# Kernel tuning notes

Hardware: AMD Instinct MI355X
Metric: run time of the kernel (lower is better)

## Reference

```python
import jax, jax.numpy as jnp
import numpy as np

D_IN = 768
D_OUT = 768
NUM_HEADS = 12
HEAD_DIM = D_OUT // NUM_HEADS


def setup_inputs() -> dict:
    key = jax.random.key(0)
    ks = jax.random.split(key, 6)
    s = 1.0 / np.sqrt(D_IN)
    X = jax.random.normal(ks[0], (4, 2048, D_IN), dtype=jnp.float32)
    Wq = jax.random.uniform(ks[1], (D_IN, D_OUT), jnp.float32, -s, s)
    Wk = jax.random.uniform(ks[2], (D_IN, D_OUT), jnp.float32, -s, s)
    Wv = jax.random.uniform(ks[3], (D_IN, D_OUT), jnp.float32, -s, s)
    Wo = jax.random.uniform(ks[4], (D_OUT, D_OUT), jnp.float32, -s, s)
    bo = jax.random.uniform(ks[5], (D_OUT,), jnp.float32, -s, s)
    return {"X": X, "Wq": Wq, "Wk": Wk, "Wv": Wv, "Wo": Wo, "bo": bo}


def reference(X, Wq, Wk, Wv, Wo, bo):
    b, n, _ = X.shape
    # QKV projections, split heads -> [b, h, n, d]
    def split(t):
        return t.reshape(b, n, NUM_HEADS, HEAD_DIM).transpose(0, 2, 1, 3)
    q = split(X @ Wq)
    k = split(X @ Wk)
    v = split(X @ Wv)
    scores = jnp.einsum('bhqd,bhkd->bhqk', q, k) / np.sqrt(HEAD_DIM).astype(np.float32)
    causal = jnp.triu(jnp.ones((n, n), dtype=bool), k=1)
    scores = jnp.where(causal, -jnp.inf, scores)
    attn = jax.nn.softmax(scores, axis=-1)  # dropout p=0 -> identity
    ctx = jnp.einsum('bhqk,bhkd->bhqd', attn, v)
    ctx = ctx.transpose(0, 2, 1, 3).reshape(b, n, D_OUT)
    return ctx @ Wo + bo
```

## Files before the change

kernel.cpp:

```cpp
#include <hip/hip_runtime.h>
#include <stdint.h>

#define B_  4
#define N_  2048
#define D_  768
#define H_  12
#define HD_ 64
#define M_  (B_*N_)

typedef short bf8 __attribute__((ext_vector_type(8)));
typedef float f32x4 __attribute__((ext_vector_type(4)));

static __device__ __forceinline__ unsigned short f2bf(float f) {
    unsigned u = __float_as_uint(f);
    unsigned r = u + 0x7fffu + ((u >> 16) & 1u);
    return (unsigned short)(r >> 16);
}

static __device__ __forceinline__ unsigned pk2bf(float f0, float f1) {
    return ((__float_as_uint(f1) + 0x8000u) & 0xFFFF0000u) |
           ((__float_as_uint(f0) + 0x8000u) >> 16);
}

#if __has_builtin(__builtin_amdgcn_exp2f)
#define EXP2(x) __builtin_amdgcn_exp2f(x)
#else
#define EXP2(x) exp2f(x)
#endif

#define GLOAD_LDS16(gptr, lptr)                                                   \
    __builtin_amdgcn_global_load_lds(                                             \
        (const __attribute__((address_space(1))) void*)(gptr),                    \
        (__attribute__((address_space(3))) void*)(lptr), 16, 0, 0)

#define QSCALE 0.1803368801111204f

__global__ __launch_bounds__(256) void convert_x(const float* __restrict__ X,
                                                 unsigned short* __restrict__ Xb) {
    const size_t i = ((size_t)blockIdx.x * 256 + threadIdx.x) * 8;
    const float4 a = *(const float4*)(X + i);
    const float4 b = *(const float4*)(X + i + 4);
    ushort4 lo, hi;
    lo.x = f2bf(a.x); lo.y = f2bf(a.y); lo.z = f2bf(a.z); lo.w = f2bf(a.w);
    hi.x = f2bf(b.x); hi.y = f2bf(b.y); hi.z = f2bf(b.z); hi.w = f2bf(b.w);
    *(ushort4*)(Xb + i)     = lo;
    *(ushort4*)(Xb + i + 4) = hi;
}

__global__ __launch_bounds__(256) void transpose_w(
    const float* __restrict__ Wq, const float* __restrict__ Wk,
    const float* __restrict__ Wv, const float* __restrict__ Wo,
    unsigned short* __restrict__ Wqt, unsigned short* __restrict__ Wkt,
    unsigned short* __restrict__ Wvt, unsigned short* __restrict__ Wot)
{
    __shared__ float tile[32][33];
    const int z = blockIdx.z;
    const float* W = (z == 0) ? Wq : (z == 1) ? Wk : (z == 2) ? Wv : Wo;
    unsigned short* Wt = (z == 0) ? Wqt : (z == 1) ? Wkt : (z == 2) ? Wvt : Wot;
    const int k0 = blockIdx.x * 32, n0 = blockIdx.y * 32;
    const int tx = threadIdx.x & 31, ty = threadIdx.x >> 5;
    #pragma unroll
    for (int i = 0; i < 4; ++i)
        tile[ty + 8 * i][tx] = W[(size_t)(k0 + ty + 8 * i) * D_ + n0 + tx];
    __syncthreads();
    #pragma unroll
    for (int i = 0; i < 4; ++i)
        Wt[(size_t)(n0 + ty + 8 * i) * D_ + k0 + tx] = f2bf(tile[tx][ty + 8 * i]);
}

__global__ __launch_bounds__(256) void qkv_mfma(
    const unsigned short* __restrict__ Xb,
    const unsigned short* __restrict__ Wqt, const unsigned short* __restrict__ Wkt,
    const unsigned short* __restrict__ Wvt,
    unsigned short* __restrict__ Qb, unsigned short* __restrict__ Kb,
    unsigned short* __restrict__ Vt)
{
    __shared__ unsigned short As[2][8192];
    __shared__ unsigned short Bs[2][8192];

    const int t = threadIdx.x;
    const int wave = t >> 6, lane = t & 63;
    const int col = lane & 15, quad = lane >> 4;
    const int wm = (wave & 1) * 64, wn = (wave >> 1) * 64;

    const int orig = blockIdx.x;
    const int wgid = (orig & 7) * 144 + (orig >> 3);
    const int m0  = (wgid / 18) * 128;
    const int nm  = wgid % 18;
    const int mat = nm / 6;
    const int n0  = (nm % 6) * 128;
    const unsigned short* Wt = (mat == 0) ? Wqt : (mat == 1) ? Wkt : Wvt;
    const bool sw = (mat != 2);

    const unsigned short* Ag = Xb + (size_t)(m0 + (t >> 2)) * D_ + (t & 3) * 8;
    const unsigned short* Bg = Wt + (size_t)(n0 + (t >> 2)) * D_ + (t & 3) * 8;
    unsigned short* AsD = &As[0][0] + t * 8;
    unsigned short* BsD = &Bs[0][0] + t * 8;

#define QKV_STAGE(bsel, kk)                                                        \
    do {                                                                           \
        GLOAD_LDS16(Ag + (kk),                        AsD + (bsel) * 8192);        \
        GLOAD_LDS16(Ag + (kk) + 32,                   AsD + (bsel) * 8192 + 4096); \
        GLOAD_LDS16(Ag + (size_t)64 * D_ + (kk),      AsD + (bsel) * 8192 + 2048); \
        GLOAD_LDS16(Ag + (size_t)64 * D_ + (kk) + 32, AsD + (bsel) * 8192 + 6144); \
        GLOAD_LDS16(Bg + (kk),                        BsD + (bsel) * 8192);        \
        GLOAD_LDS16(Bg + (kk) + 32,                   BsD + (bsel) * 8192 + 4096); \
        GLOAD_LDS16(Bg + (size_t)64 * D_ + (kk),      BsD + (bsel) * 8192 + 2048); \
        GLOAD_LDS16(Bg + (size_t)64 * D_ + (kk) + 32, BsD + (bsel) * 8192 + 6144); \
    } while (0)

    f32x4 acc[4][4] = {};

    QKV_STAGE(0, 0);
    asm volatile("s_waitcnt vmcnt(0)" ::: "memory");
    __builtin_amdgcn_s_barrier();
    __builtin_amdgcn_sched_barrier(0);

    #pragma unroll 2
    for (int it = 0; it < 12; ++it) {
        const int cur = it & 1;
        if (it + 1 < 12) QKV_STAGE(cur ^ 1, (it + 1) * 64);

        const unsigned short* Ab = &As[cur][0];
        const unsigned short* Bb = &Bs[cur][0];
        #pragma unroll
        for (int ks = 0; ks < 2; ++ks) {
            bf8 a[4], b[4];
            #pragma unroll
            for (int i = 0; i < 4; ++i)
                a[i] = *(const bf8*)(Ab + ks * 4096 + (wm + i * 16 + col) * 32 + quad * 8);
            #pragma unroll
            for (int j = 0; j < 4; ++j)
                b[j] = *(const bf8*)(Bb + ks * 4096 + (wn + j * 16 + col) * 32 + quad * 8);
            if (sw) {
                #pragma unroll
                for (int i = 0; i < 4; ++i)
                    #pragma unroll
                    for (int j = 0; j < 4; ++j)
                        acc[i][j] = __builtin_amdgcn_mfma_f32_16x16x32_bf16(b[j], a[i], acc[i][j], 0, 0, 0);
            } else {
                #pragma unroll
                for (int i = 0; i < 4; ++i)
                    #pragma unroll
                    for (int j = 0; j < 4; ++j)
                        acc[i][j] = __builtin_amdgcn_mfma_f32_16x16x32_bf16(a[i], b[j], acc[i][j], 0, 0, 0);
            }
        }

        asm volatile("s_waitcnt vmcnt(0)" ::: "memory");
        __builtin_amdgcn_s_barrier();
        __builtin_amdgcn_sched_barrier(0);
    }
#undef QKV_STAGE

    if (sw) {
        unsigned short* Out = (mat == 0) ? Qb : Kb;
        const float qsc = (mat == 0) ? QSCALE : 1.0f;
        #pragma unroll
        for (int i = 0; i < 4; ++i) {
            const int token = m0 + wm + i * 16 + col;
            const int bb = token >> 11, nn = token & (N_ - 1);
            #pragma unroll
            for (int j = 0; j < 4; ++j) {
                const int n = n0 + wn + j * 16 + quad * 4;
                const int h = n >> 6, d = n & 63;
                ushort4 pk;
                pk.x = f2bf(acc[i][j][0] * qsc);
                pk.y = f2bf(acc[i][j][1] * qsc);
                pk.z = f2bf(acc[i][j][2] * qsc);
                pk.w = f2bf(acc[i][j][3] * qsc);
                *(ushort4*)(Out + ((size_t)(bb * H_ + h) * N_ + nn) * HD_ + d) = pk;
            }
        }
    } else {
        #pragma unroll
        for (int j = 0; j < 4; ++j) {
            const int n = n0 + wn + j * 16 + col;
            const int h = n >> 6, d = n & 63;
            #pragma unroll
            for (int i = 0; i < 4; ++i) {
                const int mb = m0 + wm + i * 16 + quad * 4;
                const int bb = mb >> 11;
                const int nn = mb & (N_ - 1);
                const int nnp = (nn & ~31) | ((quad >> 1) << 4) | ((quad & 1) << 3) |
                                ((i & 1) << 2);
                ushort4 pk;
                pk.x = f2bf(acc[i][j][0]); pk.y = f2bf(acc[i][j][1]);
                pk.z = f2bf(acc[i][j][2]); pk.w = f2bf(acc[i][j][3]);
                *(ushort4*)(Vt + ((size_t)(bb * H_ + h) * HD_ + d) * N_ + nnp) = pk;
            }
        }
    }
}

static __device__ __forceinline__ void qk_mfma8(
    const bf8 (&ka)[4][2], bf8 qb0, bf8 qb1, f32x4 (&s)[4])
{
    __builtin_amdgcn_s_setprio(1);
    #pragma unroll
    for (int kc = 0; kc < 4; ++kc) {
        s[kc] = __builtin_amdgcn_mfma_f32_16x16x32_bf16(ka[kc][0], qb0, s[kc], 0, 0, 0);
        s[kc] = __builtin_amdgcn_mfma_f32_16x16x32_bf16(ka[kc][1], qb1, s[kc], 0, 0, 0);
    }
    __builtin_amdgcn_s_setprio(0);
}

static __device__ __forceinline__ void softmax_pack(
    const f32x4 (&s)[4], int k0, int q, bool mask, float& lpart,
    bf8& pb0, bf8& pb1, int quad)
{
    float p[4][4];
    if (mask) {
        #pragma unroll
        for (int kc = 0; kc < 4; ++kc)
            #pragma unroll
            for (int r = 0; r < 4; ++r) {
                const int key = k0 + kc * 16 + quad * 4 + r;
                p[kc][r] = EXP2((key > q) ? -INFINITY : s[kc][r]);
            }
    } else {
        #pragma unroll
        for (int kc = 0; kc < 4; ++kc)
            #pragma unroll
            for (int r = 0; r < 4; ++r) p[kc][r] = EXP2(s[kc][r]);
    }

    #pragma unroll
    for (int kc = 0; kc < 4; ++kc)
        #pragma unroll
        for (int r = 0; r < 4; ++r) lpart += p[kc][r];

    uint4 u0, u1;
    u0.x = pk2bf(p[0][0], p[0][1]); u0.y = pk2bf(p[0][2], p[0][3]);
    u0.z = pk2bf(p[1][0], p[1][1]); u0.w = pk2bf(p[1][2], p[1][3]);
    u1.x = pk2bf(p[2][0], p[2][1]); u1.y = pk2bf(p[2][2], p[2][3]);
    u1.z = pk2bf(p[3][0], p[3][1]); u1.w = pk2bf(p[3][2], p[3][3]);
    pb0 = *(bf8*)&u0;
    pb1 = *(bf8*)&u1;
}

static __device__ __forceinline__ void pv_acc(
    bf8 pb0, bf8 pb1, const bf8 (&va)[4][2], f32x4 (&o)[4])
{
    __builtin_amdgcn_s_setprio(1);
    #pragma unroll
    for (int dc = 0; dc < 4; ++dc) {
        o[dc] = __builtin_amdgcn_mfma_f32_16x16x32_bf16(va[dc][0], pb0, o[dc], 0, 0, 0);
        o[dc] = __builtin_amdgcn_mfma_f32_16x16x32_bf16(va[dc][1], pb1, o[dc], 0, 0, 0);
    }
    __builtin_amdgcn_s_setprio(0);
}

__global__ __launch_bounds__(256, 3) void attn_mfma(
    const unsigned short* __restrict__ Qb,
    const unsigned short* __restrict__ Kb,
    const unsigned short* __restrict__ Vt,
    unsigned short* __restrict__ Ctxb)
{
    __shared__ unsigned short Kl[2][64 * 64];
    __shared__ unsigned short Vl[2][64 * 64];

    const int t = threadIdx.x;
    const int wave = t >> 6;
    const int lane = t & 63;
    const int col  = lane & 15;
    const int quad = lane >> 4;

    const int orig = blockIdx.x;
    const int bid  = (orig & 7) * 96 + (orig >> 3);
    const int bh  = bid >> 4;
    const int x   = bid & 15;
    const int tl  = x, th = 31 - x;
    const int q0L = tl * 64 + wave * 16;
    const int q0H = th * 64 + wave * 16;
    const int qL  = q0L + col;
    const int qH  = q0H + col;

    const unsigned short* Kp = Kb + (size_t)bh * N_ * HD_;
    const unsigned short* Vp = Vt + (size_t)bh * HD_ * N_;
    const unsigned short* QpL = Qb + ((size_t)bh * N_ + q0L) * HD_;
    const unsigned short* QpH = Qb + ((size_t)bh * N_ + q0H) * HD_;

    const bf8 qbL0 = *(const bf8*)(QpL + (size_t)col * HD_ + quad * 8);
    const bf8 qbL1 = *(const bf8*)(QpL + (size_t)col * HD_ + 32 + quad * 8);
    const bf8 qbH0 = *(const bf8*)(QpH + (size_t)col * HD_ + quad * 8);
    const bf8 qbH1 = *(const bf8*)(QpH + (size_t)col * HD_ + 32 + quad * 8);

    f32x4 oL[4] = {}, oH[4] = {};
    float lL = 0.f, lH = 0.f;

    const int srow = t >> 3;
    const int gcol = (t & 7) ^ (srow & 7);
    const unsigned short* Kg = Kp + (size_t)srow * HD_ + gcol * 8;
    const unsigned short* Vg = Vp + (size_t)srow * N_ + gcol * 8;
    unsigned short* KlD = &Kl[0][0] + t * 8;
    unsigned short* VlD = &Vl[0][0] + t * 8;

#define ATT_STAGE(bsel, kt_)                                                       \
    do {                                                                           \
        GLOAD_LDS16(Kg + (size_t)(kt_) * 64 * HD_,        KlD + (bsel) * 4096);    \
        GLOAD_LDS16(Kg + (size_t)((kt_) * 64 + 32) * HD_, KlD + (bsel) * 4096 + 2048); \
        GLOAD_LDS16(Vg + (kt_) * 64,                      VlD + (bsel) * 4096);    \
        GLOAD_LDS16(Vg + (size_t)32 * N_ + (kt_) * 64,    VlD + (bsel) * 4096 + 2048); \
    } while (0)

    const int iters = 32 - x;

    const int rd0 = ((quad    ) ^ (col & 7)) * 8;
    const int rd1 = ((quad + 4) ^ (col & 7)) * 8;

    ATT_STAGE(0, 0);

    for (int kt = 0; kt < iters; ++kt) {
        const int k0 = kt * 64;
        const bool actL = (kt <= tl);
        const int cur = kt & 1;

        asm volatile("s_waitcnt vmcnt(0)" ::: "memory");
        __builtin_amdgcn_s_barrier();
        __builtin_amdgcn_sched_barrier(0);

        if (kt + 1 < iters) ATT_STAGE(cur ^ 1, kt + 1);

        const unsigned short* Kc = &Kl[cur][0];
        const unsigned short* Vc = &Vl[cur][0];

        bf8 ka[4][2];
        #pragma unroll
        for (int kc = 0; kc < 4; ++kc) {
            const unsigned short* kr = Kc + (kc * 16 + col) * 64;
            ka[kc][0] = *(const bf8*)(kr + rd0);
            ka[kc][1] = *(const bf8*)(kr + rd1);
        }
        bf8 va[4][2];
        #pragma unroll
        for (int dc = 0; dc < 4; ++dc) {
            const unsigned short* vr = Vc + (dc * 16 + col) * 64;
            va[dc][0] = *(const bf8*)(vr + rd0);
            va[dc][1] = *(const bf8*)(vr + rd1);
        }

        f32x4 sH[4] = {};
        qk_mfma8(ka, qbH0, qbH1, sH);
        f32x4 sL[4] = {};
        if (actL) qk_mfma8(ka, qbL0, qbL1, sL);

        bf8 pbH0, pbH1;
        softmax_pack(sH, k0, qH, kt == th, lH, pbH0, pbH1, quad);
        pv_acc(pbH0, pbH1, va, oH);

        if (actL) {
            bf8 pbL0, pbL1;
            softmax_pack(sL, k0, qL, kt == tl, lL, pbL0, pbL1, quad);
            pv_acc(pbL0, pbL1, va, oL);
        }
    }
#undef ATT_STAGE

    const int b = bh / H_;
    const int h = bh % H_;
    {
        float l = lH;
        l += __shfl_xor(l, 16, 64);
        l += __shfl_xor(l, 32, 64);
        const float inv = 1.0f / l;
        unsigned short* cp = Ctxb + ((size_t)(b * N_ + qH)) * D_ + h * HD_;
        #pragma unroll
        for (int dc = 0; dc < 4; ++dc) {
            uint2 pk;
            pk.x = pk2bf(oH[dc][0] * inv, oH[dc][1] * inv);
            pk.y = pk2bf(oH[dc][2] * inv, oH[dc][3] * inv);
            *(uint2*)(cp + dc * 16 + quad * 4) = pk;
        }
    }
    {
        float l = lL;
        l += __shfl_xor(l, 16, 64);
        l += __shfl_xor(l, 32, 64);
        const float inv = 1.0f / l;
        unsigned short* cp = Ctxb + ((size_t)(b * N_ + qL)) * D_ + h * HD_;
        #pragma unroll
        for (int dc = 0; dc < 4; ++dc) {
            uint2 pk;
            pk.x = pk2bf(oL[dc][0] * inv, oL[dc][1] * inv);
            pk.y = pk2bf(oL[dc][2] * inv, oL[dc][3] * inv);
            *(uint2*)(cp + dc * 16 + quad * 4) = pk;
        }
    }
}

__global__ __launch_bounds__(256) void out_mfma(
    const unsigned short* __restrict__ Ctxb,
    const unsigned short* __restrict__ Wot,
    const float* __restrict__ bo,
    float* __restrict__ Out)
{
    __shared__ unsigned short As[2][8192];
    __shared__ unsigned short Bs[2][8192];

    const int t = threadIdx.x;
    const int wave = t >> 6, lane = t & 63;
    const int col = lane & 15, quad = lane >> 4;
    const int wm = (wave & 1) * 64, wn = (wave >> 1) * 64;

    const int orig = blockIdx.x;
    const int wgid = (orig & 7) * 48 + (orig >> 3);
    const int m0 = (wgid / 6) * 128;
    const int n0 = (wgid % 6) * 128;

    const unsigned short* Ag = Ctxb + (size_t)(m0 + (t >> 2)) * D_ + (t & 3) * 8;
    const unsigned short* Bg = Wot + (size_t)(n0 + (t >> 2)) * D_ + (t & 3) * 8;
    unsigned short* AsD = &As[0][0] + t * 8;
    unsigned short* BsD = &Bs[0][0] + t * 8;

#define OUT_STAGE(bsel, kk)                                                        \
    do {                                                                           \
        GLOAD_LDS16(Ag + (kk),                        AsD + (bsel) * 8192);        \
        GLOAD_LDS16(Ag + (kk) + 32,                   AsD + (bsel) * 8192 + 4096); \
        GLOAD_LDS16(Ag + (size_t)64 * D_ + (kk),      AsD + (bsel) * 8192 + 2048); \
        GLOAD_LDS16(Ag + (size_t)64 * D_ + (kk) + 32, AsD + (bsel) * 8192 + 6144); \
        GLOAD_LDS16(Bg + (kk),                        BsD + (bsel) * 8192);        \
        GLOAD_LDS16(Bg + (kk) + 32,                   BsD + (bsel) * 8192 + 4096); \
        GLOAD_LDS16(Bg + (size_t)64 * D_ + (kk),      BsD + (bsel) * 8192 + 2048); \
        GLOAD_LDS16(Bg + (size_t)64 * D_ + (kk) + 32, BsD + (bsel) * 8192 + 6144); \
    } while (0)

    f32x4 acc[4][4] = {};

    OUT_STAGE(0, 0);
    asm volatile("s_waitcnt vmcnt(0)" ::: "memory");
    __builtin_amdgcn_s_barrier();
    __builtin_amdgcn_sched_barrier(0);

    #pragma unroll 2
    for (int it = 0; it < 12; ++it) {
        const int cur = it & 1;
        if (it + 1 < 12) OUT_STAGE(cur ^ 1, (it + 1) * 64);

        const unsigned short* Ab = &As[cur][0];
        const unsigned short* Bb = &Bs[cur][0];
        #pragma unroll
        for (int ks = 0; ks < 2; ++ks) {
            bf8 a[4], b[4];
            #pragma unroll
            for (int i = 0; i < 4; ++i)
                a[i] = *(const bf8*)(Ab + ks * 4096 + (wm + i * 16 + col) * 32 + quad * 8);
            #pragma unroll
            for (int j = 0; j < 4; ++j)
                b[j] = *(const bf8*)(Bb + ks * 4096 + (wn + j * 16 + col) * 32 + quad * 8);
            #pragma unroll
            for (int i = 0; i < 4; ++i)
                #pragma unroll
                for (int j = 0; j < 4; ++j)
                    acc[i][j] = __builtin_amdgcn_mfma_f32_16x16x32_bf16(b[j], a[i], acc[i][j], 0, 0, 0);
        }

        asm volatile("s_waitcnt vmcnt(0)" ::: "memory");
        __builtin_amdgcn_s_barrier();
        __builtin_amdgcn_sched_barrier(0);
    }
#undef OUT_STAGE

    #pragma unroll
    for (int i = 0; i < 4; ++i) {
        const int m = m0 + wm + i * 16 + col;
        #pragma unroll
        for (int j = 0; j < 4; ++j) {
            const int n = n0 + wn + j * 16 + quad * 4;
            const float4 bias = *(const float4*)(bo + n);
            float4 o;
            o.x = acc[i][j][0] + bias.x;
            o.y = acc[i][j][1] + bias.y;
            o.z = acc[i][j][2] + bias.z;
            o.w = acc[i][j][3] + bias.w;
            *(float4*)(Out + (size_t)m * D_ + n) = o;
        }
    }
}

extern "C" void kernel_launch(void* const* d_in, const int* in_sizes, int n_in,
                              void* d_out, int out_size, void* d_ws, size_t ws_size,
                              hipStream_t stream) {
    const float* X  = (const float*)d_in[0];
    const float* Wq = (const float*)d_in[1];
    const float* Wk = (const float*)d_in[2];
    const float* Wv = (const float*)d_in[3];
    const float* Wo = (const float*)d_in[4];
    const float* bo = (const float*)d_in[5];
    float* out = (float*)d_out;

    const size_t elems = (size_t)M_ * D_;
    const size_t welems = (size_t)D_ * D_;
    unsigned short* Xb  = (unsigned short*)d_ws;
    unsigned short* Wqt = Xb + elems;
    unsigned short* Wkt = Wqt + welems;
    unsigned short* Wvt = Wkt + welems;
    unsigned short* Wot = Wvt + welems;
    unsigned short* Qb  = Wot + welems;
    unsigned short* Kb  = Qb + elems;
    unsigned short* Vt  = Kb + elems;
    unsigned short* Ctxb = Xb;

    convert_x<<<dim3(elems / 2048), 256, 0, stream>>>(X, Xb);
    transpose_w<<<dim3(24, 24, 4), 256, 0, stream>>>(Wq, Wk, Wv, Wo, Wqt, Wkt, Wvt, Wot);

    qkv_mfma<<<dim3(1152), 256, 0, stream>>>(Xb, Wqt, Wkt, Wvt, Qb, Kb, Vt);

    attn_mfma<<<dim3(B_ * H_ * 16), 256, 0, stream>>>(Qb, Kb, Vt, Ctxb);

    out_mfma<<<dim3(384), 256, 0, stream>>>(Ctxb, Wot, bo, out);
}
```

Measured before the change: 199.6 us.

## Use four-stage K=32 LDS pipeline with partial vmcnt waits in projection GEMMs

Replaces the double-buffered K=64 staging in the QKV and output projection GEMMs with a four-buffer ring of K=32 slices, keeping three slices of global-to-LDS loads in flight. Partial vmcnt waits replace full drains, so more memory latency can be hidden behind MFMA work. In exchange, the number of barriers doubles and each compute step between barriers is smaller.

```diff
diff --git a/kernel.cpp b/kernel.cpp
--- a/kernel.cpp
+++ b/kernel.cpp
@@ -75,8 +75,8 @@
     unsigned short* __restrict__ Qb, unsigned short* __restrict__ Kb,
     unsigned short* __restrict__ Vt)
 {
-    __shared__ unsigned short As[2][8192];
-    __shared__ unsigned short Bs[2][8192];
+    __shared__ unsigned short As[4][4096];
+    __shared__ unsigned short Bs[4][4096];
 
     const int t = threadIdx.x;
     const int wave = t >> 6, lane = t & 63;
@@ -94,64 +94,66 @@
 
     const unsigned short* Ag = Xb + (size_t)(m0 + (t >> 2)) * D_ + (t & 3) * 8;
     const unsigned short* Bg = Wt + (size_t)(n0 + (t >> 2)) * D_ + (t & 3) * 8;
-    unsigned short* AsD = &As[0][0] + t * 8;
-    unsigned short* BsD = &Bs[0][0] + t * 8;
-
-#define QKV_STAGE(bsel, kk)                                                        \
-    do {                                                                           \
-        GLOAD_LDS16(Ag + (kk),                        AsD + (bsel) * 8192);        \
-        GLOAD_LDS16(Ag + (kk) + 32,                   AsD + (bsel) * 8192 + 4096); \
-        GLOAD_LDS16(Ag + (size_t)64 * D_ + (kk),      AsD + (bsel) * 8192 + 2048); \
-        GLOAD_LDS16(Ag + (size_t)64 * D_ + (kk) + 32, AsD + (bsel) * 8192 + 6144); \
-        GLOAD_LDS16(Bg + (kk),                        BsD + (bsel) * 8192);        \
-        GLOAD_LDS16(Bg + (kk) + 32,                   BsD + (bsel) * 8192 + 4096); \
-        GLOAD_LDS16(Bg + (size_t)64 * D_ + (kk),      BsD + (bsel) * 8192 + 2048); \
-        GLOAD_LDS16(Bg + (size_t)64 * D_ + (kk) + 32, BsD + (bsel) * 8192 + 6144); \
+
+#define QKV_STAGE_P(bsel, p)                                                      \
+    do {                                                                          \
+        GLOAD_LDS16(Ag + (p) * 32,                     &As[bsel][0] + t * 8);     \
+        GLOAD_LDS16(Ag + (size_t)64 * D_ + (p) * 32,   &As[bsel][0] + 2048 + t * 8); \
+        GLOAD_LDS16(Bg + (p) * 32,                     &Bs[bsel][0] + t * 8);     \
+        GLOAD_LDS16(Bg + (size_t)64 * D_ + (p) * 32,   &Bs[bsel][0] + 2048 + t * 8); \
     } while (0)
 
     f32x4 acc[4][4] = {};
 
-    QKV_STAGE(0, 0);
+#define QKV_COMP(bsel)                                                            \
+    do {                                                                          \
+        const unsigned short* Ab = &As[bsel][0];                                  \
+        const unsigned short* Bb = &Bs[bsel][0];                                  \
+        bf8 a[4], b[4];                                                           \
+        _Pragma("unroll")                                                         \
+        for (int i = 0; i < 4; ++i)                                               \
+            a[i] = *(const bf8*)(Ab + (wm + i * 16 + col) * 32 + quad * 8);       \
+        _Pragma("unroll")                                                         \
+        for (int j = 0; j < 4; ++j)                                               \
+            b[j] = *(const bf8*)(Bb + (wn + j * 16 + col) * 32 + quad * 8);       \
+        if (sw) {                                                                 \
+            _Pragma("unroll")                                                     \
+            for (int i = 0; i < 4; ++i)                                           \
+                _Pragma("unroll")                                                 \
+                for (int j = 0; j < 4; ++j)                                       \
+                    acc[i][j] = __builtin_amdgcn_mfma_f32_16x16x32_bf16(          \
+                        b[j], a[i], acc[i][j], 0, 0, 0);                          \
+        } else {                                                                  \
+            _Pragma("unroll")                                                     \
+            for (int i = 0; i < 4; ++i)                                           \
+                _Pragma("unroll")                                                 \
+                for (int j = 0; j < 4; ++j)                                       \
+                    acc[i][j] = __builtin_amdgcn_mfma_f32_16x16x32_bf16(          \
+                        a[i], b[j], acc[i][j], 0, 0, 0);                          \
+        }                                                                         \
+    } while (0)
+
+    QKV_STAGE_P(0, 0);
+    QKV_STAGE_P(1, 1);
+    QKV_STAGE_P(2, 2);
+
+    for (int p = 0; p < 22; ++p) {
+        asm volatile("s_waitcnt vmcnt(8)" ::: "memory");
+        __builtin_amdgcn_s_barrier();
+        __builtin_amdgcn_sched_barrier(0);
+        if (p < 21) QKV_STAGE_P((p + 3) & 3, p + 3);
+        QKV_COMP(p & 3);
+    }
+    asm volatile("s_waitcnt vmcnt(4)" ::: "memory");
+    __builtin_amdgcn_s_barrier();
+    __builtin_amdgcn_sched_barrier(0);
+    QKV_COMP(2);
     asm volatile("s_waitcnt vmcnt(0)" ::: "memory");
     __builtin_amdgcn_s_barrier();
     __builtin_amdgcn_sched_barrier(0);
-
-    #pragma unroll 2
-    for (int it = 0; it < 12; ++it) {
-        const int cur = it & 1;
-        if (it + 1 < 12) QKV_STAGE(cur ^ 1, (it + 1) * 64);
-
-        const unsigned short* Ab = &As[cur][0];
-        const unsigned short* Bb = &Bs[cur][0];
-        #pragma unroll
-        for (int ks = 0; ks < 2; ++ks) {
-            bf8 a[4], b[4];
-            #pragma unroll
-            for (int i = 0; i < 4; ++i)
-                a[i] = *(const bf8*)(Ab + ks * 4096 + (wm + i * 16 + col) * 32 + quad * 8);
-            #pragma unroll
-            for (int j = 0; j < 4; ++j)
-                b[j] = *(const bf8*)(Bb + ks * 4096 + (wn + j * 16 + col) * 32 + quad * 8);
-            if (sw) {
-                #pragma unroll
-                for (int i = 0; i < 4; ++i)
-                    #pragma unroll
-                    for (int j = 0; j < 4; ++j)
-                        acc[i][j] = __builtin_amdgcn_mfma_f32_16x16x32_bf16(b[j], a[i], acc[i][j], 0, 0, 0);
-            } else {
-                #pragma unroll
-                for (int i = 0; i < 4; ++i)
-                    #pragma unroll
-                    for (int j = 0; j < 4; ++j)
-                        acc[i][j] = __builtin_amdgcn_mfma_f32_16x16x32_bf16(a[i], b[j], acc[i][j], 0, 0, 0);
-            }
-        }
-
-        asm volatile("s_waitcnt vmcnt(0)" ::: "memory");
-        __builtin_amdgcn_s_barrier();
-        __builtin_amdgcn_sched_barrier(0);
-    }
-#undef QKV_STAGE
+    QKV_COMP(3);
+#undef QKV_STAGE_P
+#undef QKV_COMP
 
     if (sw) {
         unsigned short* Out = (mat == 0) ? Qb : Kb;
@@ -395,8 +397,8 @@
     const float* __restrict__ bo,
     float* __restrict__ Out)
 {
-    __shared__ unsigned short As[2][8192];
-    __shared__ unsigned short Bs[2][8192];
+    __shared__ unsigned short As[4][4096];
+    __shared__ unsigned short Bs[4][4096];
 
     const int t = threadIdx.x;
     const int wave = t >> 6, lane = t & 63;
@@ -410,56 +412,57 @@
 
     const unsigned short* Ag = Ctxb + (size_t)(m0 + (t >> 2)) * D_ + (t & 3) * 8;
     const unsigned short* Bg = Wot + (size_t)(n0 + (t >> 2)) * D_ + (t & 3) * 8;
-    unsigned short* AsD = &As[0][0] + t * 8;
-    unsigned short* BsD = &Bs[0][0] + t * 8;
-
-#define OUT_STAGE(bsel, kk)                                                        \
-    do {                                                                           \
-        GLOAD_LDS16(Ag + (kk),                        AsD + (bsel) * 8192);        \
-        GLOAD_LDS16(Ag + (kk) + 32,                   AsD + (bsel) * 8192 + 4096); \
-        GLOAD_LDS16(Ag + (size_t)64 * D_ + (kk),      AsD + (bsel) * 8192 + 2048); \
-        GLOAD_LDS16(Ag + (size_t)64 * D_ + (kk) + 32, AsD + (bsel) * 8192 + 6144); \
-        GLOAD_LDS16(Bg + (kk),                        BsD + (bsel) * 8192);        \
-        GLOAD_LDS16(Bg + (kk) + 32,                   BsD + (bsel) * 8192 + 4096); \
-        GLOAD_LDS16(Bg + (size_t)64 * D_ + (kk),      BsD + (bsel) * 8192 + 2048); \
-        GLOAD_LDS16(Bg + (size_t)64 * D_ + (kk) + 32, BsD + (bsel) * 8192 + 6144); \
+
+#define OUT_STAGE_P(bsel, p)                                                      \
+    do {                                                                          \
+        GLOAD_LDS16(Ag + (p) * 32,                     &As[bsel][0] + t * 8);     \
+        GLOAD_LDS16(Ag + (size_t)64 * D_ + (p) * 32,   &As[bsel][0] + 2048 + t * 8); \
+        GLOAD_LDS16(Bg + (p) * 32,                     &Bs[bsel][0] + t * 8);     \
+        GLOAD_LDS16(Bg + (size_t)64 * D_ + (p) * 32,   &Bs[bsel][0] + 2048 + t * 8); \
     } while (0)
 
     f32x4 acc[4][4] = {};
 
-    OUT_STAGE(0, 0);
+#define OUT_COMP(bsel)                                                            \
+    do {                                                                          \
+        const unsigned short* Ab = &As[bsel][0];                                  \
+        const unsigned short* Bb = &Bs[bsel][0];                                  \
+        bf8 a[4], b[4];                                                           \
+        _Pragma("unroll")                                                         \
+        for (int i = 0; i < 4; ++i)                                               \
+            a[i] = *(const bf8*)(Ab + (wm + i * 16 + col) * 32 + quad * 8);       \
+        _Pragma("unroll")                                                         \
+        for (int j = 0; j < 4; ++j)                                               \
+            b[j] = *(const bf8*)(Bb + (wn + j * 16 + col) * 32 + quad * 8);       \
+        _Pragma("unroll")                                                         \
+        for (int i = 0; i < 4; ++i)                                               \
+            _Pragma("unroll")                                                     \
+            for (int j = 0; j < 4; ++j)                                           \
+                acc[i][j] = __builtin_amdgcn_mfma_f32_16x16x32_bf16(              \
+                    b[j], a[i], acc[i][j], 0, 0, 0);                              \
+    } while (0)
+
+    OUT_STAGE_P(0, 0);
+    OUT_STAGE_P(1, 1);
+    OUT_STAGE_P(2, 2);
+
+    for (int p = 0; p < 22; ++p) {
+        asm volatile("s_waitcnt vmcnt(8)" ::: "memory");
+        __builtin_amdgcn_s_barrier();
+        __builtin_amdgcn_sched_barrier(0);
+        if (p < 21) OUT_STAGE_P((p + 3) & 3, p + 3);
+        OUT_COMP(p & 3);
+    }
+    asm volatile("s_waitcnt vmcnt(4)" ::: "memory");
+    __builtin_amdgcn_s_barrier();
+    __builtin_amdgcn_sched_barrier(0);
+    OUT_COMP(2);
     asm volatile("s_waitcnt vmcnt(0)" ::: "memory");
     __builtin_amdgcn_s_barrier();
     __builtin_amdgcn_sched_barrier(0);
-
-    #pragma unroll 2
-    for (int it = 0; it < 12; ++it) {
-        const int cur = it & 1;
-        if (it + 1 < 12) OUT_STAGE(cur ^ 1, (it + 1) * 64);
-
-        const unsigned short* Ab = &As[cur][0];
-        const unsigned short* Bb = &Bs[cur][0];
-        #pragma unroll
-        for (int ks = 0; ks < 2; ++ks) {
-            bf8 a[4], b[4];
-            #pragma unroll
-            for (int i = 0; i < 4; ++i)
-                a[i] = *(const bf8*)(Ab + ks * 4096 + (wm + i * 16 + col) * 32 + quad * 8);
-            #pragma unroll
-            for (int j = 0; j < 4; ++j)
-                b[j] = *(const bf8*)(Bb + ks * 4096 + (wn + j * 16 + col) * 32 + quad * 8);
-            #pragma unroll
-            for (int i = 0; i < 4; ++i)
-                #pragma unroll
-                for (int j = 0; j < 4; ++j)
-                    acc[i][j] = __builtin_amdgcn_mfma_f32_16x16x32_bf16(b[j], a[i], acc[i][j], 0, 0, 0);
-        }
-
-        asm volatile("s_waitcnt vmcnt(0)" ::: "memory");
-        __builtin_amdgcn_s_barrier();
-        __builtin_amdgcn_sched_barrier(0);
-    }
-#undef OUT_STAGE
+    OUT_COMP(3);
+#undef OUT_STAGE_P
+#undef OUT_COMP
 
     #pragma unroll
     for (int i = 0; i < 4; ++i) {
```

Result: slower. 219.8 us (+10.1%).

## Merge prep kernels and use 512-thread QKV GEMM blocks with smaller wave tiles

Applied to the files above, without the earlier changes.

Fuses the X conversion and the weight transpose into a single prep launch, which saves one kernel launch. The QKV GEMM now runs 512 threads per block: eight waves each compute a 64x32 sub-tile instead of four waves doing 64x64, and each thread issues half as many async global-to-LDS loads per stage. This aims for more waves in flight and fewer accumulator registers per wave. The cost is more LDS fragment reloads per MFMA and more waves contending at barriers.

```diff
diff --git a/kernel.cpp b/kernel.cpp
--- a/kernel.cpp
+++ b/kernel.cpp
@@ -35,40 +35,44 @@
 
 #define QSCALE 0.1803368801111204f
 
-__global__ __launch_bounds__(256) void convert_x(const float* __restrict__ X,
-                                                 unsigned short* __restrict__ Xb) {
-    const size_t i = ((size_t)blockIdx.x * 256 + threadIdx.x) * 8;
-    const float4 a = *(const float4*)(X + i);
-    const float4 b = *(const float4*)(X + i + 4);
-    ushort4 lo, hi;
-    lo.x = f2bf(a.x); lo.y = f2bf(a.y); lo.z = f2bf(a.z); lo.w = f2bf(a.w);
-    hi.x = f2bf(b.x); hi.y = f2bf(b.y); hi.z = f2bf(b.z); hi.w = f2bf(b.w);
-    *(ushort4*)(Xb + i)     = lo;
-    *(ushort4*)(Xb + i + 4) = hi;
-}
-
-__global__ __launch_bounds__(256) void transpose_w(
+__global__ __launch_bounds__(256) void prep(
+    const float* __restrict__ X,
     const float* __restrict__ Wq, const float* __restrict__ Wk,
     const float* __restrict__ Wv, const float* __restrict__ Wo,
+    unsigned short* __restrict__ Xb,
     unsigned short* __restrict__ Wqt, unsigned short* __restrict__ Wkt,
     unsigned short* __restrict__ Wvt, unsigned short* __restrict__ Wot)
 {
     __shared__ float tile[32][33];
-    const int z = blockIdx.z;
-    const float* W = (z == 0) ? Wq : (z == 1) ? Wk : (z == 2) ? Wv : Wo;
-    unsigned short* Wt = (z == 0) ? Wqt : (z == 1) ? Wkt : (z == 2) ? Wvt : Wot;
-    const int k0 = blockIdx.x * 32, n0 = blockIdx.y * 32;
-    const int tx = threadIdx.x & 31, ty = threadIdx.x >> 5;
-    #pragma unroll
-    for (int i = 0; i < 4; ++i)
-        tile[ty + 8 * i][tx] = W[(size_t)(k0 + ty + 8 * i) * D_ + n0 + tx];
-    __syncthreads();
-    #pragma unroll
-    for (int i = 0; i < 4; ++i)
-        Wt[(size_t)(n0 + ty + 8 * i) * D_ + k0 + tx] = f2bf(tile[tx][ty + 8 * i]);
-}
-
-__global__ __launch_bounds__(256) void qkv_mfma(
+    const int bid = blockIdx.x;
+    if (bid < 3072) {
+        const size_t i = ((size_t)bid * 256 + threadIdx.x) * 8;
+        const float4 a = *(const float4*)(X + i);
+        const float4 b = *(const float4*)(X + i + 4);
+        ushort4 lo, hi;
+        lo.x = f2bf(a.x); lo.y = f2bf(a.y); lo.z = f2bf(a.z); lo.w = f2bf(a.w);
+        hi.x = f2bf(b.x); hi.y = f2bf(b.y); hi.z = f2bf(b.z); hi.w = f2bf(b.w);
+        *(ushort4*)(Xb + i)     = lo;
+        *(ushort4*)(Xb + i + 4) = hi;
+    } else {
+        const int r = bid - 3072;
+        const int z = r / 576;
+        const int rem = r % 576;
+        const float* W = (z == 0) ? Wq : (z == 1) ? Wk : (z == 2) ? Wv : Wo;
+        unsigned short* Wt = (z == 0) ? Wqt : (z == 1) ? Wkt : (z == 2) ? Wvt : Wot;
+        const int k0 = (rem % 24) * 32, n0 = (rem / 24) * 32;
+        const int tx = threadIdx.x & 31, ty = threadIdx.x >> 5;
+        #pragma unroll
+        for (int i = 0; i < 4; ++i)
+            tile[ty + 8 * i][tx] = W[(size_t)(k0 + ty + 8 * i) * D_ + n0 + tx];
+        __syncthreads();
+        #pragma unroll
+        for (int i = 0; i < 4; ++i)
+            Wt[(size_t)(n0 + ty + 8 * i) * D_ + k0 + tx] = f2bf(tile[tx][ty + 8 * i]);
+    }
+}
+
+__global__ __launch_bounds__(512) void qkv_mfma(
     const unsigned short* __restrict__ Xb,
     const unsigned short* __restrict__ Wqt, const unsigned short* __restrict__ Wkt,
     const unsigned short* __restrict__ Wvt,
@@ -81,7 +85,8 @@
     const int t = threadIdx.x;
     const int wave = t >> 6, lane = t & 63;
     const int col = lane & 15, quad = lane >> 4;
-    const int wm = (wave & 1) * 64, wn = (wave >> 1) * 64;
+    const int wm = (wave & 1) * 64;
+    const int wn = (wave >> 1) * 32;
 
     const int orig = blockIdx.x;
     const int wgid = (orig & 7) * 144 + (orig >> 3);
@@ -94,22 +99,16 @@
 
     const unsigned short* Ag = Xb + (size_t)(m0 + (t >> 2)) * D_ + (t & 3) * 8;
     const unsigned short* Bg = Wt + (size_t)(n0 + (t >> 2)) * D_ + (t & 3) * 8;
-    unsigned short* AsD = &As[0][0] + t * 8;
-    unsigned short* BsD = &Bs[0][0] + t * 8;
-
-#define QKV_STAGE(bsel, kk)                                                        \
-    do {                                                                           \
-        GLOAD_LDS16(Ag + (kk),                        AsD + (bsel) * 8192);        \
-        GLOAD_LDS16(Ag + (kk) + 32,                   AsD + (bsel) * 8192 + 4096); \
-        GLOAD_LDS16(Ag + (size_t)64 * D_ + (kk),      AsD + (bsel) * 8192 + 2048); \
-        GLOAD_LDS16(Ag + (size_t)64 * D_ + (kk) + 32, AsD + (bsel) * 8192 + 6144); \
-        GLOAD_LDS16(Bg + (kk),                        BsD + (bsel) * 8192);        \
-        GLOAD_LDS16(Bg + (kk) + 32,                   BsD + (bsel) * 8192 + 4096); \
-        GLOAD_LDS16(Bg + (size_t)64 * D_ + (kk),      BsD + (bsel) * 8192 + 2048); \
-        GLOAD_LDS16(Bg + (size_t)64 * D_ + (kk) + 32, BsD + (bsel) * 8192 + 6144); \
+
+#define QKV_STAGE(bsel, kk)                                                       \
+    do {                                                                          \
+        GLOAD_LDS16(Ag + (kk),      &As[bsel][0] + t * 8);                        \
+        GLOAD_LDS16(Ag + (kk) + 32, &As[bsel][0] + 4096 + t * 8);                 \
+        GLOAD_LDS16(Bg + (kk),      &Bs[bsel][0] + t * 8);                        \
+        GLOAD_LDS16(Bg + (kk) + 32, &Bs[bsel][0] + 4096 + t * 8);                 \
     } while (0)
 
-    f32x4 acc[4][4] = {};
+    f32x4 acc[4][2] = {};
 
     QKV_STAGE(0, 0);
     asm volatile("s_waitcnt vmcnt(0)" ::: "memory");
@@ -125,24 +124,24 @@
         const unsigned short* Bb = &Bs[cur][0];
         #pragma unroll
         for (int ks = 0; ks < 2; ++ks) {
-            bf8 a[4], b[4];
+            bf8 a[4], b[2];
             #pragma unroll
             for (int i = 0; i < 4; ++i)
                 a[i] = *(const bf8*)(Ab + ks * 4096 + (wm + i * 16 + col) * 32 + quad * 8);
             #pragma unroll
-            for (int j = 0; j < 4; ++j)
+            for (int j = 0; j < 2; ++j)
                 b[j] = *(const bf8*)(Bb + ks * 4096 + (wn + j * 16 + col) * 32 + quad * 8);
             if (sw) {
                 #pragma unroll
                 for (int i = 0; i < 4; ++i)
                     #pragma unroll
-                    for (int j = 0; j < 4; ++j)
+                    for (int j = 0; j < 2; ++j)
                         acc[i][j] = __builtin_amdgcn_mfma_f32_16x16x32_bf16(b[j], a[i], acc[i][j], 0, 0, 0);
             } else {
                 #pragma unroll
                 for (int i = 0; i < 4; ++i)
                     #pragma unroll
-                    for (int j = 0; j < 4; ++j)
+                    for (int j = 0; j < 2; ++j)
                         acc[i][j] = __builtin_amdgcn_mfma_f32_16x16x32_bf16(a[i], b[j], acc[i][j], 0, 0, 0);
             }
         }
@@ -161,7 +160,7 @@
             const int token = m0 + wm + i * 16 + col;
             const int bb = token >> 11, nn = token & (N_ - 1);
             #pragma unroll
-            for (int j = 0; j < 4; ++j) {
+            for (int j = 0; j < 2; ++j) {
                 const int n = n0 + wn + j * 16 + quad * 4;
                 const int h = n >> 6, d = n & 63;
                 ushort4 pk;
@@ -174,7 +173,7 @@
         }
     } else {
         #pragma unroll
-        for (int j = 0; j < 4; ++j) {
+        for (int j = 0; j < 2; ++j) {
             const int n = n0 + wn + j * 16 + col;
             const int h = n >> 6, d = n & 63;
             #pragma unroll
@@ -501,10 +500,10 @@
     unsigned short* Vt  = Kb + elems;
     unsigned short* Ctxb = Xb;
 
-    convert_x<<<dim3(elems / 2048), 256, 0, stream>>>(X, Xb);
-    transpose_w<<<dim3(24, 24, 4), 256, 0, stream>>>(Wq, Wk, Wv, Wo, Wqt, Wkt, Wvt, Wot);
-
-    qkv_mfma<<<dim3(1152), 256, 0, stream>>>(Xb, Wqt, Wkt, Wvt, Qb, Kb, Vt);
+    prep<<<dim3(3072 + 2304), 256, 0, stream>>>(X, Wq, Wk, Wv, Wo,
+                                                Xb, Wqt, Wkt, Wvt, Wot);
+
+    qkv_mfma<<<dim3(1152), 512, 0, stream>>>(Xb, Wqt, Wkt, Wvt, Qb, Kb, Vt);
 
     attn_mfma<<<dim3(B_ * H_ * 16), 256, 0, stream>>>(Qb, Kb, Vt, Ctxb);
 
```

Result: no change. 198.9 us (-0.3%).
